# Kernel tuning notes

Measured on AMD Instinct MI355X. Metric: run time of the kernel, lower is better.

Reference implementation:

```python
import jax, jax.numpy as jnp
import numpy as np

B, T, I, H = 64, 512, 512, 512


def setup_inputs() -> dict:
    key = jax.random.key(0)
    ks = jax.random.split(key, 7)
    xavier_std = float(np.sqrt(2.0 / (B + H)))  # matches xavier_normal_ on [B,H]
    w_scale = float(1.0 / np.sqrt(H))           # ~ pytorch LSTMCell default scale
    return {
        "x": jax.random.normal(ks[0], (B, T, I), dtype=jnp.float32),
        "h0": jax.random.normal(ks[1], (B, H), dtype=jnp.float32) * xavier_std,
        "c0": jax.random.normal(ks[2], (B, H), dtype=jnp.float32) * xavier_std,
        "W_ih": jax.random.normal(ks[3], (4 * H, I), dtype=jnp.float32) * w_scale,
        "W_hh": jax.random.normal(ks[4], (4 * H, H), dtype=jnp.float32) * w_scale,
        "b_ih": jax.random.normal(ks[5], (4 * H,), dtype=jnp.float32) * w_scale,
        "b_hh": jax.random.normal(ks[6], (4 * H,), dtype=jnp.float32) * w_scale,
    }


def lstm_forward(x, h0, c0, W_ih, W_hh, b_ih, b_hh):
    # Precompute the input-to-gate projection for all timesteps in one big GEMM.
    # xg: [T, B, 4H]
    xg = jnp.einsum("bti,gi->tbg", x, W_ih) + (b_ih + b_hh)

    def step(carry, xg_t):
        h, c = carry
        gates = xg_t + h @ W_hh.T  # [B, 4H]
        i, f, g, o = jnp.split(gates, 4, axis=-1)
        i = jax.nn.sigmoid(i)
        f = jax.nn.sigmoid(f)
        g = jnp.tanh(g)
        o = jax.nn.sigmoid(o)
        c = f * c + i * g
        h = o * jnp.tanh(c)
        return (h, c), h

    (h_T, c_T), outs = jax.lax.scan(step, (h0, c0), xg)
    output = jnp.transpose(outs, (1, 0, 2))  # [B, T, H]
    return output, h_T, c_T


def reference(x, h0, c0, W_ih, W_hh, b_ih, b_hh):
    return lstm_forward(x, h0, c0, W_ih, W_hh, b_ih, b_hh)
```

## Files before the change

kernel.cpp:

```cpp
#include <hip/hip_runtime.h>
#include <hip/hip_fp16.h>
#include <string.h>

constexpr int B = 64, T = 512, I = 512, H = 512, G = 2048;

typedef _Float16 half8 __attribute__((ext_vector_type(8)));
typedef float floatx4 __attribute__((ext_vector_type(4)));

__global__ __launch_bounds__(256, 2) void xg_gemm(
    const float* __restrict__ x,
    const float* __restrict__ W_ih,
    const float* __restrict__ b_ih,
    const float* __restrict__ b_hh,
    _Float16* __restrict__ xg)
{
    const int tid  = threadIdx.x;
    const int wave = tid >> 6, lane = tid & 63;
    const int quad = lane >> 4, col = lane & 15;
    const int rowA = blockIdx.x * 128 + wave * 16;
    const int rowB = rowA + 64;

    __shared__ __align__(16) _Float16 xs[64][264];

    half8 wfA[16], wfB[16];
    {
        const float* wpA = W_ih + (size_t)(rowA + col) * I;
        const float* wpB = W_ih + (size_t)(rowB + col) * I;
#pragma unroll
        for (int kc = 0; kc < 16; ++kc) {
            half8 vA, vB;
#pragma unroll
            for (int j = 0; j < 8; ++j) {
                vA[j] = (_Float16)wpA[kc * 32 + quad * 8 + j];
                vB[j] = (_Float16)wpB[kc * 32 + quad * 8 + j];
            }
            wfA[kc] = vA; wfB[kc] = vB;
        }
    }
    float biasA[4], biasB[4];
#pragma unroll
    for (int r = 0; r < 4; ++r) {
        biasA[r] = b_ih[rowA + quad * 4 + r] + b_hh[rowA + quad * 4 + r];
        biasB[r] = b_ih[rowB + quad * 4 + r] + b_hh[rowB + quad * 4 + r];
    }

    for (int ti = 0; ti < 4; ++ti) {
        const int t = blockIdx.y * 4 + ti;
        floatx4 accA[4], accB[4];
#pragma unroll
        for (int nt = 0; nt < 4; ++nt) {
            accA[nt] = (floatx4){0.f, 0.f, 0.f, 0.f};
            accB[nt] = (floatx4){0.f, 0.f, 0.f, 0.f};
        }

        for (int hfl = 0; hfl < 2; ++hfl) {
            __syncthreads();
#pragma unroll 4
            for (int c = 0; c < 16; ++c) {
                int idx = c * 256 + tid;
                int row = idx >> 6;
                int kk  = (idx & 63) * 4;
                const float4 v = *(const float4*)(x + ((size_t)row * T + t) * I + hfl * 256 + kk);
                xs[row][kk + 0] = (_Float16)v.x;
                xs[row][kk + 1] = (_Float16)v.y;
                xs[row][kk + 2] = (_Float16)v.z;
                xs[row][kk + 3] = (_Float16)v.w;
            }
            __syncthreads();
#pragma unroll
            for (int kc = 0; kc < 8; ++kc) {
#pragma unroll
                for (int nt = 0; nt < 4; ++nt) {
                    const half8 bfr = *(const half8*)&xs[nt * 16 + col][kc * 32 + quad * 8];
                    accA[nt] = __builtin_amdgcn_mfma_f32_16x16x32_f16(
                        wfA[hfl * 8 + kc], bfr, accA[nt], 0, 0, 0);
                    accB[nt] = __builtin_amdgcn_mfma_f32_16x16x32_f16(
                        wfB[hfl * 8 + kc], bfr, accB[nt], 0, 0, 0);
                }
            }
        }
#pragma unroll
        for (int nt = 0; nt < 4; ++nt) {
            int b = nt * 16 + col;
#pragma unroll
            for (int r = 0; r < 4; ++r) {
                xg[((size_t)t * G + rowA + quad * 4 + r) * B + b] = (_Float16)(accA[nt][r] + biasA[r]);
                xg[((size_t)t * G + rowB + quad * 4 + r) * B + b] = (_Float16)(accB[nt][r] + biasB[r]);
            }
        }
    }
}

__global__ __launch_bounds__(256, 1) void lstm_rec(
    const float* __restrict__ h0,
    const float* __restrict__ c0,
    const float* __restrict__ W_hh,
    const _Float16* __restrict__ xg,
    _Float16* __restrict__ hbuf,
    unsigned int* __restrict__ cnt,
    float* __restrict__ out)
{
    const int s   = blockIdx.x;
    const int hs  = s * 8;
    const int tid = threadIdx.x;
    const int wave = tid >> 6, lane = tid & 63;
    const int quad = lane >> 4, col = lane & 15;
    const int b = wave * 16 + col;

    int arow0 = (col < 8) ? (hs + col) : (512 + hs + col - 8);
    int arow1 = arow0 + 1024;
    half8 wf0[16], wf1[16];
#pragma unroll
    for (int kc = 0; kc < 16; ++kc) {
        const float* p0 = W_hh + (size_t)arow0 * H + kc * 32 + quad * 8;
        const float* p1 = W_hh + (size_t)arow1 * H + kc * 32 + quad * 8;
        half8 v0, v1;
#pragma unroll
        for (int j = 0; j < 8; ++j) { v0[j] = (_Float16)p0[j]; v1[j] = (_Float16)p1[j]; }
        wf0[kc] = v0; wf1[kc] = v1;
    }

    int xrow0[4], xrow1[4];
#pragma unroll
    for (int r = 0; r < 4; ++r) {
        int lr = quad * 4 + r;
        xrow0[r] = (lr < 8) ? (hs + lr) : (512 + hs + lr - 8);
        xrow1[r] = xrow0[r] + 1024;
    }

    float c[4];
#pragma unroll
    for (int r = 0; r < 4; ++r) {
        int jj = (quad & 1) * 4 + r;
        c[r] = c0[(size_t)b * H + hs + jj];
    }

    if (quad < 2) {
        _Float16 v4[4];
#pragma unroll
        for (int r = 0; r < 4; ++r)
            v4[r] = (_Float16)h0[(size_t)b * H + hs + (quad & 1) * 4 + r];
        unsigned long long uv; __builtin_memcpy(&uv, v4, 8);
        __hip_atomic_store((unsigned long long*)(hbuf + (size_t)b * H + hs + (quad & 1) * 4),
                           uv, __ATOMIC_RELAXED, __HIP_MEMORY_SCOPE_AGENT);
    }
    asm volatile("s_waitcnt vmcnt(0)" ::: "memory");
    __syncthreads();
    if (tid == 0)
        __hip_atomic_fetch_add(cnt, 1u, __ATOMIC_RELAXED, __HIP_MEMORY_SCOPE_AGENT);

    float xp0[4], xp1[4];
#pragma unroll
    for (int r = 0; r < 4; ++r) {
        xp0[r] = (float)xg[(size_t)xrow0[r] * B + b];
        xp1[r] = (float)xg[(size_t)xrow1[r] * B + b];
    }

    while (__hip_atomic_load(cnt, __ATOMIC_RELAXED, __HIP_MEMORY_SCOPE_AGENT) < 64u) {}
    asm volatile("" ::: "memory");

    float hh[4] = {0.f, 0.f, 0.f, 0.f};

    for (int t = 0; t < T; ++t) {
        const _Float16* hcur = hbuf + (size_t)(t & 1) * B * H;
        _Float16*       hnxt = hbuf + (size_t)((t + 1) & 1) * B * H;

        unsigned long long hu0[16], hu1[16];
#pragma unroll
        for (int kc = 0; kc < 16; ++kc) {
            unsigned long long* hp =
                (unsigned long long*)(hcur + (size_t)b * H + kc * 32 + quad * 8);
            hu0[kc] = __hip_atomic_load(hp,     __ATOMIC_RELAXED, __HIP_MEMORY_SCOPE_AGENT);
            hu1[kc] = __hip_atomic_load(hp + 1, __ATOMIC_RELAXED, __HIP_MEMORY_SCOPE_AGENT);
        }

        floatx4 acc0 = (floatx4){0.f, 0.f, 0.f, 0.f};
        floatx4 acc1 = (floatx4){0.f, 0.f, 0.f, 0.f};
#pragma unroll
        for (int kc = 0; kc < 16; ++kc) {
            half8 bfr;
            __builtin_memcpy(&bfr, &hu0[kc], 8);
            __builtin_memcpy((char*)&bfr + 8, &hu1[kc], 8);
            acc0 = __builtin_amdgcn_mfma_f32_16x16x32_f16(wf0[kc], bfr, acc0, 0, 0, 0);
            acc1 = __builtin_amdgcn_mfma_f32_16x16x32_f16(wf1[kc], bfr, acc1, 0, 0, 0);
        }

        float p0[4], p1[4];
#pragma unroll
        for (int r = 0; r < 4; ++r) {
            p0[r] = acc0[r] + xp0[r];
            p1[r] = acc1[r] + xp1[r];
        }
        float e0[4], e1[4];
#pragma unroll
        for (int r = 0; r < 4; ++r) {
            e0[r] = __shfl_xor(p0[r], 32);
            e1[r] = __shfl_xor(p1[r], 32);
        }
#pragma unroll
        for (int r = 0; r < 4; ++r) {
            float iv = (quad < 2) ? p0[r] : e0[r];
            float fv = (quad < 2) ? e0[r] : p0[r];
            float gv = (quad < 2) ? p1[r] : e1[r];
            float ov = (quad < 2) ? e1[r] : p1[r];
            float ii = 1.f / (1.f + __expf(-iv));
            float ff = 1.f / (1.f + __expf(-fv));
            float eg = __expf(-2.f * gv);
            float gg = (1.f - eg) / (1.f + eg);
            float oo = 1.f / (1.f + __expf(-ov));
            float cn = ff * c[r] + ii * gg;
            c[r] = cn;
            float ec = __expf(-2.f * cn);
            hh[r] = oo * ((1.f - ec) / (1.f + ec));
        }
        if (quad < 2) {
            _Float16 v4[4] = {(_Float16)hh[0], (_Float16)hh[1],
                              (_Float16)hh[2], (_Float16)hh[3]};
            unsigned long long uv; __builtin_memcpy(&uv, v4, 8);
            __hip_atomic_store((unsigned long long*)(hnxt + (size_t)b * H + hs + (quad & 1) * 4),
                               uv, __ATOMIC_RELAXED, __HIP_MEMORY_SCOPE_AGENT);
            float* op = out + ((size_t)b * T + t) * H + hs + (quad & 1) * 4;
            op[0] = hh[0]; op[1] = hh[1]; op[2] = hh[2]; op[3] = hh[3];
        }

        asm volatile("s_waitcnt vmcnt(0)" ::: "memory");
        __syncthreads();
        if (tid == 0)
            __hip_atomic_fetch_add(cnt, 1u, __ATOMIC_RELAXED, __HIP_MEMORY_SCOPE_AGENT);

        if (t + 1 < T) {
            const _Float16* xgt = xg + (size_t)(t + 1) * G * B;
#pragma unroll
            for (int r = 0; r < 4; ++r) {
                xp0[r] = (float)xgt[(size_t)xrow0[r] * B + b];
                xp1[r] = (float)xgt[(size_t)xrow1[r] * B + b];
            }
        }

        const unsigned int tgt = 64u * (unsigned)(t + 2);
        while (__hip_atomic_load(cnt, __ATOMIC_RELAXED, __HIP_MEMORY_SCOPE_AGENT) < tgt) {}
        asm volatile("" ::: "memory");
    }

    if (quad < 2) {
        float* hT = out + (size_t)B * T * H;
        float* cT = hT + (size_t)B * H;
#pragma unroll
        for (int r = 0; r < 4; ++r) {
            int jj = (quad & 1) * 4 + r;
            hT[(size_t)b * H + hs + jj] = hh[r];
            cT[(size_t)b * H + hs + jj] = c[r];
        }
    }
}

extern "C" void kernel_launch(void* const* d_in, const int* in_sizes, int n_in,
                              void* d_out, int out_size, void* d_ws, size_t ws_size,
                              hipStream_t stream) {
    const float* x    = (const float*)d_in[0];
    const float* h0   = (const float*)d_in[1];
    const float* c0   = (const float*)d_in[2];
    const float* W_ih = (const float*)d_in[3];
    const float* W_hh = (const float*)d_in[4];
    const float* b_ih = (const float*)d_in[5];
    const float* b_hh = (const float*)d_in[6];
    float* out = (float*)d_out;

    unsigned int* cnt = (unsigned int*)d_ws;
    _Float16* hbuf = (_Float16*)((char*)d_ws + 1024);
    _Float16* xg   = (_Float16*)((char*)d_ws + 1024 + (size_t)2 * B * H * 2);

    hipMemsetAsync(d_ws, 0, 1024, stream);

    xg_gemm<<<dim3(16, 128), 256, 0, stream>>>(x, W_ih, b_ih, b_hh, xg);
    lstm_rec<<<64, 256, 0, stream>>>(h0, c0, W_hh, xg, hbuf, cnt, out);
}
```

Measured before the change: 3.492 ms.

## Replace atomic counter grid barrier with per-wave flag array polled by lanes

Each wave now publishes its own step number to a per-wave flag slot instead of doing a block-wide __syncthreads plus one atomic add to a shared counter. Every lane polls four flags with two 64-bit loads and the wave exits the spin when all 256 flags reach the target. This removes the contended atomic RMW and the intra-block barrier. The change also prefetches the next step's xg values before the MFMA loop and moves the output stores after the flag publish, so less work sits on the critical path. In exchange, polling traffic grows because every lane now reads flags, and correctness depends on relaxed ordering plus vmcnt waits.

```diff
diff --git a/kernel.cpp b/kernel.cpp
--- a/kernel.cpp
+++ b/kernel.cpp
@@ -97,7 +97,7 @@
     const float* __restrict__ W_hh,
     const _Float16* __restrict__ xg,
     _Float16* __restrict__ hbuf,
-    unsigned int* __restrict__ cnt,
+    unsigned int* __restrict__ flags,
     float* __restrict__ out)
 {
     const int s   = blockIdx.x;
@@ -106,6 +106,7 @@
     const int wave = tid >> 6, lane = tid & 63;
     const int quad = lane >> 4, col = lane & 15;
     const int b = wave * 16 + col;
+    const int gwave = s * 4 + wave;
 
     int arow0 = (col < 8) ? (hs + col) : (512 + hs + col - 8);
     int arow1 = arow0 + 1024;
@@ -145,9 +146,8 @@
                            uv, __ATOMIC_RELAXED, __HIP_MEMORY_SCOPE_AGENT);
     }
     asm volatile("s_waitcnt vmcnt(0)" ::: "memory");
-    __syncthreads();
-    if (tid == 0)
-        __hip_atomic_fetch_add(cnt, 1u, __ATOMIC_RELAXED, __HIP_MEMORY_SCOPE_AGENT);
+    if (lane == 0)
+        __hip_atomic_store(flags + gwave, 1u, __ATOMIC_RELAXED, __HIP_MEMORY_SCOPE_AGENT);
 
     float xp0[4], xp1[4];
 #pragma unroll
@@ -156,8 +156,19 @@
         xp1[r] = (float)xg[(size_t)xrow1[r] * B + b];
     }
 
-    while (__hip_atomic_load(cnt, __ATOMIC_RELAXED, __HIP_MEMORY_SCOPE_AGENT) < 64u) {}
+    const unsigned long long* fq = (const unsigned long long*)flags;
+#define POLL_FLAGS(tgtval)                                                           \
+    for (;;) {                                                                       \
+        unsigned long long fa = __hip_atomic_load(fq + 2 * lane,     __ATOMIC_RELAXED, __HIP_MEMORY_SCOPE_AGENT); \
+        unsigned long long fb = __hip_atomic_load(fq + 2 * lane + 1, __ATOMIC_RELAXED, __HIP_MEMORY_SCOPE_AGENT); \
+        unsigned m0 = (unsigned)fa, m1 = (unsigned)(fa >> 32);                       \
+        unsigned m2 = (unsigned)fb, m3 = (unsigned)(fb >> 32);                       \
+        unsigned mn = min(min(m0, m1), min(m2, m3));                                 \
+        if (__all(mn >= (tgtval))) break;                                            \
+    }                                                                                \
     asm volatile("" ::: "memory");
+
+    POLL_FLAGS(1u)
 
     float hh[4] = {0.f, 0.f, 0.f, 0.f};
 
@@ -172,6 +183,16 @@
                 (unsigned long long*)(hcur + (size_t)b * H + kc * 32 + quad * 8);
             hu0[kc] = __hip_atomic_load(hp,     __ATOMIC_RELAXED, __HIP_MEMORY_SCOPE_AGENT);
             hu1[kc] = __hip_atomic_load(hp + 1, __ATOMIC_RELAXED, __HIP_MEMORY_SCOPE_AGENT);
+        }
+
+        float xn0[4], xn1[4];
+        if (t + 1 < T) {
+            const _Float16* xgt = xg + (size_t)(t + 1) * G * B;
+#pragma unroll
+            for (int r = 0; r < 4; ++r) {
+                xn0[r] = (float)xgt[(size_t)xrow0[r] * B + b];
+                xn1[r] = (float)xgt[(size_t)xrow1[r] * B + b];
+            }
         }
 
         floatx4 acc0 = (floatx4){0.f, 0.f, 0.f, 0.f};
@@ -219,27 +240,25 @@
             unsigned long long uv; __builtin_memcpy(&uv, v4, 8);
             __hip_atomic_store((unsigned long long*)(hnxt + (size_t)b * H + hs + (quad & 1) * 4),
                                uv, __ATOMIC_RELAXED, __HIP_MEMORY_SCOPE_AGENT);
+        }
+
+        asm volatile("s_waitcnt vmcnt(0)" ::: "memory");
+        if (lane == 0)
+            __hip_atomic_store(flags + gwave, (unsigned)(t + 2),
+                               __ATOMIC_RELAXED, __HIP_MEMORY_SCOPE_AGENT);
+
+        if (quad < 2) {
             float* op = out + ((size_t)b * T + t) * H + hs + (quad & 1) * 4;
             op[0] = hh[0]; op[1] = hh[1]; op[2] = hh[2]; op[3] = hh[3];
         }
 
-        asm volatile("s_waitcnt vmcnt(0)" ::: "memory");
-        __syncthreads();
-        if (tid == 0)
-            __hip_atomic_fetch_add(cnt, 1u, __ATOMIC_RELAXED, __HIP_MEMORY_SCOPE_AGENT);
+#pragma unroll
+        for (int r = 0; r < 4; ++r) { xp0[r] = xn0[r]; xp1[r] = xn1[r]; }
 
         if (t + 1 < T) {
-            const _Float16* xgt = xg + (size_t)(t + 1) * G * B;
-#pragma unroll
-            for (int r = 0; r < 4; ++r) {
-                xp0[r] = (float)xgt[(size_t)xrow0[r] * B + b];
-                xp1[r] = (float)xgt[(size_t)xrow1[r] * B + b];
-            }
-        }
-
-        const unsigned int tgt = 64u * (unsigned)(t + 2);
-        while (__hip_atomic_load(cnt, __ATOMIC_RELAXED, __HIP_MEMORY_SCOPE_AGENT) < tgt) {}
-        asm volatile("" ::: "memory");
+            const unsigned tgt = (unsigned)(t + 2);
+            POLL_FLAGS(tgt)
+        }
     }
 
     if (quad < 2) {
@@ -252,6 +271,7 @@
             cT[(size_t)b * H + hs + jj] = c[r];
         }
     }
+#undef POLL_FLAGS
 }
 
 extern "C" void kernel_launch(void* const* d_in, const int* in_sizes, int n_in,
@@ -266,12 +286,12 @@
     const float* b_hh = (const float*)d_in[6];
     float* out = (float*)d_out;
 
-    unsigned int* cnt = (unsigned int*)d_ws;
-    _Float16* hbuf = (_Float16*)((char*)d_ws + 1024);
-    _Float16* xg   = (_Float16*)((char*)d_ws + 1024 + (size_t)2 * B * H * 2);
-
-    hipMemsetAsync(d_ws, 0, 1024, stream);
+    unsigned int* flags = (unsigned int*)d_ws;
+    _Float16* hbuf = (_Float16*)((char*)d_ws + 2048);
+    _Float16* xg   = (_Float16*)((char*)d_ws + 2048 + (size_t)2 * B * H * 2);
+
+    hipMemsetAsync(d_ws, 0, 2048, stream);
 
     xg_gemm<<<dim3(16, 128), 256, 0, stream>>>(x, W_ih, b_ih, b_hh, xg);
-    lstm_rec<<<64, 256, 0, stream>>>(h0, c0, W_hh, xg, hbuf, cnt, out);
+    lstm_rec<<<64, 256, 0, stream>>>(h0, c0, W_hh, xg, hbuf, flags, out);
 }
```

Measured after the change: 5.046 ms. 1.45x slower.

## Split recurrent grid into four independent batch groups with separate barriers

Applied to the files above, without the earlier changes.

The recurrent kernel's 64 blocks are regrouped so each block handles 16 batch rows and 32 hidden units, not all 64 batch rows and 8 hidden units. Since batch rows are independent, each group of 16 blocks only needs to sync with itself. It therefore uses its own counter and hidden-state buffer, and the grid-wide barrier becomes four 16-block barriers. The final redundant wait after the last step is also skipped. This aims to cut per-step barrier latency and contention, at the cost of each block reading the full W_hh slice for more hidden rows across fewer batch columns.

```diff
diff --git a/kernel.cpp b/kernel.cpp
--- a/kernel.cpp
+++ b/kernel.cpp
@@ -97,17 +97,22 @@
     const float* __restrict__ W_hh,
     const _Float16* __restrict__ xg,
     _Float16* __restrict__ hbuf,
-    unsigned int* __restrict__ cnt,
+    unsigned int* __restrict__ cnts,
     float* __restrict__ out)
 {
-    const int s   = blockIdx.x;
-    const int hs  = s * 8;
-    const int tid = threadIdx.x;
+    const int blk  = blockIdx.x;
+    const int bg   = blk & 3;
+    const int hg   = blk >> 2;
+    const int tid  = threadIdx.x;
     const int wave = tid >> 6, lane = tid & 63;
     const int quad = lane >> 4, col = lane & 15;
-    const int b = wave * 16 + col;
-
-    int arow0 = (col < 8) ? (hs + col) : (512 + hs + col - 8);
+
+    const int bglob = bg * 16 + col;
+    const int hbase = hg * 32 + wave * 8;
+
+    unsigned int* cnt = cnts + bg * 64;
+
+    int arow0 = (col < 8) ? (hbase + col) : (512 + hbase + col - 8);
     int arow1 = arow0 + 1024;
     half8 wf0[16], wf1[16];
 #pragma unroll
@@ -124,24 +129,25 @@
 #pragma unroll
     for (int r = 0; r < 4; ++r) {
         int lr = quad * 4 + r;
-        xrow0[r] = (lr < 8) ? (hs + lr) : (512 + hs + lr - 8);
+        xrow0[r] = (lr < 8) ? (hbase + lr) : (512 + hbase + lr - 8);
         xrow1[r] = xrow0[r] + 1024;
     }
 
     float c[4];
 #pragma unroll
-    for (int r = 0; r < 4; ++r) {
-        int jj = (quad & 1) * 4 + r;
-        c[r] = c0[(size_t)b * H + hs + jj];
-    }
+    for (int r = 0; r < 4; ++r)
+        c[r] = c0[(size_t)bglob * H + hbase + (quad & 1) * 4 + r];
+
+    _Float16* hb0 = hbuf + ((size_t)0 * 4 + bg) * 16 * 512;
+    _Float16* hb1 = hbuf + ((size_t)1 * 4 + bg) * 16 * 512;
 
     if (quad < 2) {
         _Float16 v4[4];
 #pragma unroll
         for (int r = 0; r < 4; ++r)
-            v4[r] = (_Float16)h0[(size_t)b * H + hs + (quad & 1) * 4 + r];
+            v4[r] = (_Float16)h0[(size_t)bglob * H + hbase + (quad & 1) * 4 + r];
         unsigned long long uv; __builtin_memcpy(&uv, v4, 8);
-        __hip_atomic_store((unsigned long long*)(hbuf + (size_t)b * H + hs + (quad & 1) * 4),
+        __hip_atomic_store((unsigned long long*)(hb0 + (size_t)col * 512 + hbase + (quad & 1) * 4),
                            uv, __ATOMIC_RELAXED, __HIP_MEMORY_SCOPE_AGENT);
     }
     asm volatile("s_waitcnt vmcnt(0)" ::: "memory");
@@ -152,24 +158,24 @@
     float xp0[4], xp1[4];
 #pragma unroll
     for (int r = 0; r < 4; ++r) {
-        xp0[r] = (float)xg[(size_t)xrow0[r] * B + b];
-        xp1[r] = (float)xg[(size_t)xrow1[r] * B + b];
-    }
-
-    while (__hip_atomic_load(cnt, __ATOMIC_RELAXED, __HIP_MEMORY_SCOPE_AGENT) < 64u) {}
+        xp0[r] = (float)xg[(size_t)xrow0[r] * B + bglob];
+        xp1[r] = (float)xg[(size_t)xrow1[r] * B + bglob];
+    }
+
+    while (__hip_atomic_load(cnt, __ATOMIC_RELAXED, __HIP_MEMORY_SCOPE_AGENT) < 16u) {}
     asm volatile("" ::: "memory");
 
     float hh[4] = {0.f, 0.f, 0.f, 0.f};
 
     for (int t = 0; t < T; ++t) {
-        const _Float16* hcur = hbuf + (size_t)(t & 1) * B * H;
-        _Float16*       hnxt = hbuf + (size_t)((t + 1) & 1) * B * H;
+        const _Float16* hcur = (t & 1) ? hb1 : hb0;
+        _Float16*       hnxt = (t & 1) ? hb0 : hb1;
 
         unsigned long long hu0[16], hu1[16];
 #pragma unroll
         for (int kc = 0; kc < 16; ++kc) {
             unsigned long long* hp =
-                (unsigned long long*)(hcur + (size_t)b * H + kc * 32 + quad * 8);
+                (unsigned long long*)(hcur + (size_t)col * 512 + kc * 32 + quad * 8);
             hu0[kc] = __hip_atomic_load(hp,     __ATOMIC_RELAXED, __HIP_MEMORY_SCOPE_AGENT);
             hu1[kc] = __hip_atomic_load(hp + 1, __ATOMIC_RELAXED, __HIP_MEMORY_SCOPE_AGENT);
         }
@@ -217,9 +223,9 @@
             _Float16 v4[4] = {(_Float16)hh[0], (_Float16)hh[1],
                               (_Float16)hh[2], (_Float16)hh[3]};
             unsigned long long uv; __builtin_memcpy(&uv, v4, 8);
-            __hip_atomic_store((unsigned long long*)(hnxt + (size_t)b * H + hs + (quad & 1) * 4),
+            __hip_atomic_store((unsigned long long*)(hnxt + (size_t)col * 512 + hbase + (quad & 1) * 4),
                                uv, __ATOMIC_RELAXED, __HIP_MEMORY_SCOPE_AGENT);
-            float* op = out + ((size_t)b * T + t) * H + hs + (quad & 1) * 4;
+            float* op = out + ((size_t)bglob * T + t) * H + hbase + (quad & 1) * 4;
             op[0] = hh[0]; op[1] = hh[1]; op[2] = hh[2]; op[3] = hh[3];
         }
 
@@ -232,14 +238,13 @@
             const _Float16* xgt = xg + (size_t)(t + 1) * G * B;
 #pragma unroll
             for (int r = 0; r < 4; ++r) {
-                xp0[r] = (float)xgt[(size_t)xrow0[r] * B + b];
-                xp1[r] = (float)xgt[(size_t)xrow1[r] * B + b];
-            }
-        }
-
-        const unsigned int tgt = 64u * (unsigned)(t + 2);
-        while (__hip_atomic_load(cnt, __ATOMIC_RELAXED, __HIP_MEMORY_SCOPE_AGENT) < tgt) {}
-        asm volatile("" ::: "memory");
+                xp0[r] = (float)xgt[(size_t)xrow0[r] * B + bglob];
+                xp1[r] = (float)xgt[(size_t)xrow1[r] * B + bglob];
+            }
+            const unsigned int tgt = 16u * (unsigned)(t + 2);
+            while (__hip_atomic_load(cnt, __ATOMIC_RELAXED, __HIP_MEMORY_SCOPE_AGENT) < tgt) {}
+            asm volatile("" ::: "memory");
+        }
     }
 
     if (quad < 2) {
@@ -248,8 +253,8 @@
 #pragma unroll
         for (int r = 0; r < 4; ++r) {
             int jj = (quad & 1) * 4 + r;
-            hT[(size_t)b * H + hs + jj] = hh[r];
-            cT[(size_t)b * H + hs + jj] = c[r];
+            hT[(size_t)bglob * H + hbase + jj] = hh[r];
+            cT[(size_t)bglob * H + hbase + jj] = c[r];
         }
     }
 }
@@ -266,12 +271,12 @@
     const float* b_hh = (const float*)d_in[6];
     float* out = (float*)d_out;
 
-    unsigned int* cnt = (unsigned int*)d_ws;
-    _Float16* hbuf = (_Float16*)((char*)d_ws + 1024);
-    _Float16* xg   = (_Float16*)((char*)d_ws + 1024 + (size_t)2 * B * H * 2);
-
-    hipMemsetAsync(d_ws, 0, 1024, stream);
+    unsigned int* cnts = (unsigned int*)d_ws;
+    _Float16* hbuf = (_Float16*)((char*)d_ws + 2048);
+    _Float16* xg   = (_Float16*)((char*)d_ws + 2048 + (size_t)2 * 4 * 16 * 512 * 2);
+
+    hipMemsetAsync(d_ws, 0, 2048, stream);
 
     xg_gemm<<<dim3(16, 128), 256, 0, stream>>>(x, W_ih, b_ih, b_hh, xg);
-    lstm_rec<<<64, 256, 0, stream>>>(h0, c0, W_hh, xg, hbuf, cnt, out);
+    lstm_rec<<<64, 256, 0, stream>>>(h0, c0, W_hh, xg, hbuf, cnts, out);
 }
```

Measured after the change: 3.126 ms. 1.12x faster.
